# Optimization experiments

Hardware: AMD Instinct MI355X
Metric: run time of the kernel (lower is better)

## Reference

```python
import jax, jax.numpy as jnp
import numpy as np

B, NPER, H = 32, 512, 32
N, E = B * NPER, 65536
IN_CH, EDGE_CH, L1, L2, NL = 100, 16, 64, 64, 4


def setup_inputs() -> dict:
    key = jax.random.key(0)
    ks = jax.random.split(key, 14)
    f = lambda k, s: jax.random.normal(k, s, dtype=jnp.float32) * 0.1
    return {
        "x_nodes": jax.random.randint(ks[0], (N,), 0, IN_CH),
        "edge_index": jax.random.randint(ks[1], (2, E), 0, N),
        "edge_attr": jax.random.randint(ks[2], (E,), 0, EDGE_CH),
        "metal_idx": jax.random.randint(ks[3], (B,), 0, NPER),
        "loop_edge": jax.random.randint(ks[4], (B, L1, 2), 0, NPER),
        "loop_pair": jax.random.randint(ks[5], (B, L2, 2), 0, NPER),
        "node_emb": f(ks[6], (IN_CH, H)),
        "edge_emb": f(ks[7], (NL, EDGE_CH, 8)),
        "lin_w": f(ks[8], (NL, 8, H * H)),
        "lin_b": f(ks[9], (NL, H * H)),
        "root_w": f(ks[10], (NL, H, H)),
        "conv_b": f(ks[11], (NL, H)),
        "f_w": f(ks[12], (H, 1)),
        "f_b": f(ks[13], (1,)),
    }


def reference(x_nodes, edge_index, edge_attr, metal_idx, loop_edge, loop_pair,
              node_emb, edge_emb, lin_w, lin_b, root_w, conv_b, f_w, f_b):
    src, dst = edge_index[0], edge_index[1]
    # mean-aggregation denominator (clamped to 1 for isolated nodes, as PyG)
    deg = jax.ops.segment_sum(jnp.ones((E,), jnp.float32), dst, num_segments=N)
    denom = jnp.maximum(deg, 1.0)[:, None]

    x = node_emb[x_nodes]  # [N,H]
    for l in range(NL):
        # edge nn: Embedding -> ReLU -> Linear(8, H*H)
        e8 = jax.nn.relu(edge_emb[l][edge_attr])              # [E,8]
        W = (e8 @ lin_w[l] + lin_b[l]).reshape(E, H, H)       # [E,H,H]
        msg = jnp.einsum('ei,eio->eo', x[src], W)             # [E,H]
        agg = jax.ops.segment_sum(msg, dst, num_segments=N) / denom
        x_new = agg + x @ root_w[l] + conv_b[l]               # root weight + bias
        x = jax.nn.relu(x_new) if l < NL - 1 else x_new

    metal_g = metal_idx + jnp.arange(B) * NPER                # global metal node ids
    xm = x[metal_g]                                           # [B,H]
    fhM = (xm @ f_w + f_b)[:, 0]                              # [B]

    xg = x.reshape(B, NPER, H)
    bidx = jnp.arange(B)[:, None]

    def pair_prod(pairs):
        xs = xg[bidx, pairs[:, :, 0]]                         # [B,L,H]
        xt = xg[bidx, pairs[:, :, 1]]                         # [B,L,H]
        # sum(xm*xs) + sum(xm*xt) + sum(xs*(-xt))
        return jnp.sum(xm[:, None, :] * (xs + xt) - xs * xt, axis=-1)

    res_edge = pair_prod(loop_edge) - fhM[:, None]            # [B,L1]
    res_pair = -pair_prod(loop_pair)                          # [B,L2]
    return jnp.concatenate([res_edge, res_pair], axis=1)      # [B, L1+L2]
```

## Files before the change

kernel.cpp:

```cpp
#include <hip/hip_runtime.h>

#define NN 16384
#define NE 65536
#define H  32
#define BB 32
#define NPER 512
#define NL 4

__global__ void k_deg(const int* __restrict__ dst, float* __restrict__ deg) {
    int e = blockIdx.x * blockDim.x + threadIdx.x;
    if (e < NE) atomicAdd(&deg[dst[e]], 1.0f);
}

__global__ void k_embed(const int* __restrict__ x_nodes, const float* __restrict__ node_emb,
                        float* __restrict__ x) {
    int tid = blockIdx.x * blockDim.x + threadIdx.x;
    if (tid < NN * H) {
        int n = tid >> 5, h = tid & 31;
        x[tid] = node_emb[x_nodes[n] * H + h];
    }
}

__global__ void k_weights(const float* __restrict__ edge_emb_l, const float* __restrict__ lin_w_l,
                          const float* __restrict__ lin_b_l, float* __restrict__ Wt) {
    int tid = blockIdx.x * blockDim.x + threadIdx.x;
    if (tid < 16 * 1024) {
        int t = tid >> 10, io = tid & 1023;
        float acc = lin_b_l[io];
#pragma unroll
        for (int j = 0; j < 8; ++j) {
            float e = edge_emb_l[t * 8 + j];
            e = e > 0.f ? e : 0.f;
            acc += e * lin_w_l[j * 1024 + io];
        }
        Wt[tid] = acc;
    }
}

__global__ void k_msg(const int* __restrict__ src, const int* __restrict__ dst,
                      const int* __restrict__ eattr, const float* __restrict__ x,
                      const float* __restrict__ Wt, float* __restrict__ agg) {
    int tid = blockIdx.x * blockDim.x + threadIdx.x;
    int e = tid >> 5;
    int o = tid & 31;
    if (e >= NE) return;
    int s = src[e], d = dst[e], t = eattr[e];
    float xv = x[s * H + o];
    const float* __restrict__ W = Wt + t * 1024;
    int base = threadIdx.x & 32;
    float acc = 0.f;
#pragma unroll
    for (int i = 0; i < H; ++i) {
        float xi = __shfl(xv, base + i);
        acc += xi * W[i * H + o];
    }
    atomicAdd(&agg[d * H + o], acc);
}

__global__ void k_update(const float* __restrict__ x, const float* __restrict__ agg,
                         const float* __restrict__ deg, const float* __restrict__ root_w_l,
                         const float* __restrict__ conv_b_l, float* __restrict__ xout,
                         int do_relu) {
    int tid = blockIdx.x * blockDim.x + threadIdx.x;
    if (tid >= NN * H) return;
    int n = tid >> 5, o = tid & 31;
    float xv = x[tid];
    int base = threadIdx.x & 32;
    float acc = conv_b_l[o];
#pragma unroll
    for (int i = 0; i < H; ++i) {
        float xi = __shfl(xv, base + i);
        acc += xi * root_w_l[i * H + o];
    }
    float dg = deg[n];
    dg = dg < 1.f ? 1.f : dg;
    float v = agg[tid] / dg + acc;
    if (do_relu) v = v > 0.f ? v : 0.f;
    xout[tid] = v;
}

__global__ void k_final(const float* __restrict__ x, const int* __restrict__ metal_idx,
                        const int* __restrict__ loop_edge, const int* __restrict__ loop_pair,
                        const float* __restrict__ f_w, const float* __restrict__ f_b,
                        float* __restrict__ out) {
    int tid = blockIdx.x * blockDim.x + threadIdx.x;
    if (tid >= BB * 128) return;
    int b = tid >> 7, j = tid & 127;
    int mg = metal_idx[b] + b * NPER;
    const float* __restrict__ xm = x + mg * H;
    int p0, p1;
    if (j < 64) {
        p0 = loop_edge[(b * 64 + j) * 2];
        p1 = loop_edge[(b * 64 + j) * 2 + 1];
    } else {
        int j2 = j - 64;
        p0 = loop_pair[(b * 64 + j2) * 2];
        p1 = loop_pair[(b * 64 + j2) * 2 + 1];
    }
    const float* __restrict__ xs = x + (b * NPER + p0) * H;
    const float* __restrict__ xt = x + (b * NPER + p1) * H;
    float fh = f_b[0];
    float pp = 0.f;
#pragma unroll
    for (int h = 0; h < H; ++h) {
        float m = xm[h];
        fh += m * f_w[h];
        pp += m * (xs[h] + xt[h]) - xs[h] * xt[h];
    }
    out[tid] = (j < 64) ? (pp - fh) : (-pp);
}

extern "C" void kernel_launch(void* const* d_in, const int* in_sizes, int n_in,
                              void* d_out, int out_size, void* d_ws, size_t ws_size,
                              hipStream_t stream) {
    const int*   x_nodes    = (const int*)d_in[0];
    const int*   edge_index = (const int*)d_in[1];
    const int*   src        = edge_index;
    const int*   dst        = edge_index + NE;
    const int*   edge_attr  = (const int*)d_in[2];
    const int*   metal_idx  = (const int*)d_in[3];
    const int*   loop_edge  = (const int*)d_in[4];
    const int*   loop_pair  = (const int*)d_in[5];
    const float* node_emb   = (const float*)d_in[6];
    const float* edge_emb   = (const float*)d_in[7];
    const float* lin_w      = (const float*)d_in[8];
    const float* lin_b      = (const float*)d_in[9];
    const float* root_w     = (const float*)d_in[10];
    const float* conv_b     = (const float*)d_in[11];
    const float* f_w        = (const float*)d_in[12];
    const float* f_b        = (const float*)d_in[13];
    float* out = (float*)d_out;

    float* ws  = (float*)d_ws;
    float* xA  = ws;
    float* xB  = ws + NN * H;
    float* deg = ws + 2 * NN * H;
    float* Wt  = deg + NN;

    hipMemsetAsync(deg, 0, NN * sizeof(float), stream);
    k_deg<<<NE / 256, 256, 0, stream>>>(dst, deg);
    k_embed<<<NN * H / 256, 256, 0, stream>>>(x_nodes, node_emb, xA);

    float* xin = xA;
    float* xout = xB;
    for (int l = 0; l < NL; ++l) {
        k_weights<<<16 * 1024 / 256, 256, 0, stream>>>(
            edge_emb + l * 16 * 8, lin_w + l * 8 * 1024, lin_b + l * 1024, Wt);
        hipMemsetAsync(xout, 0, NN * H * sizeof(float), stream);
        k_msg<<<(NE * 32) / 256, 256, 0, stream>>>(src, dst, edge_attr, xin, Wt, xout);
        k_update<<<NN * H / 256, 256, 0, stream>>>(
            xin, xout, deg, root_w + l * H * H, conv_b + l * H, xout, l < NL - 1 ? 1 : 0);
        float* tmp = xin; xin = xout; xout = tmp;
    }

    k_final<<<(BB * 128 + 255) / 256, 256, 0, stream>>>(
        xin, metal_idx, loop_edge, loop_pair, f_w, f_b, out);
}
```

Before: 112.9 us.

## Build dst-sorted CSR once and fuse message aggregation with node update

Replaces per-layer edge-parallel atomic scatter with a CSR built once: a prep kernel fuses degree counting, embedding, and all-layer edge-weight precompute, then a single-block scan and a scatter build a destination-sorted packed edge list. Each layer becomes one kernel where a half-wave per node gathers incoming edges, applies the edge weight matrix, normalizes by degree, and adds the root transform. This removes float atomics, per-layer memsets, and several launches, but adds a serial single-block scan, and per-node work now varies with degree, so some waves sit idle while high-degree nodes finish.

```diff
diff --git a/kernel.cpp b/kernel.cpp
--- a/kernel.cpp
+++ b/kernel.cpp
@@ -7,74 +7,96 @@
 #define NPER 512
 #define NL 4
 
-__global__ void k_deg(const int* __restrict__ dst, float* __restrict__ deg) {
-    int e = blockIdx.x * blockDim.x + threadIdx.x;
-    if (e < NE) atomicAdd(&deg[dst[e]], 1.0f);
-}
+#define BLK_DEG 256
+#define BLK_EMB 2048
+#define BLK_W   256
 
-__global__ void k_embed(const int* __restrict__ x_nodes, const float* __restrict__ node_emb,
-                        float* __restrict__ x) {
-    int tid = blockIdx.x * blockDim.x + threadIdx.x;
-    if (tid < NN * H) {
+__global__ void k_prep(const int* __restrict__ dst, const int* __restrict__ x_nodes,
+                       const float* __restrict__ node_emb, const float* __restrict__ edge_emb,
+                       const float* __restrict__ lin_w, const float* __restrict__ lin_b,
+                       float* __restrict__ deg, float* __restrict__ x, float* __restrict__ Wt) {
+    int b = blockIdx.x;
+    if (b < BLK_DEG) {
+        int e = b * 256 + threadIdx.x;
+        atomicAdd(&deg[dst[e]], 1.0f);
+    } else if (b < BLK_DEG + BLK_EMB) {
+        int tid = (b - BLK_DEG) * 256 + threadIdx.x;
         int n = tid >> 5, h = tid & 31;
         x[tid] = node_emb[x_nodes[n] * H + h];
-    }
-}
-
-__global__ void k_weights(const float* __restrict__ edge_emb_l, const float* __restrict__ lin_w_l,
-                          const float* __restrict__ lin_b_l, float* __restrict__ Wt) {
-    int tid = blockIdx.x * blockDim.x + threadIdx.x;
-    if (tid < 16 * 1024) {
-        int t = tid >> 10, io = tid & 1023;
-        float acc = lin_b_l[io];
+    } else {
+        int tid = (b - BLK_DEG - BLK_EMB) * 256 + threadIdx.x;
+        int l = tid >> 14;
+        int rest = tid & 16383;
+        int t = rest >> 10, io = rest & 1023;
+        float acc = lin_b[l * 1024 + io];
 #pragma unroll
         for (int j = 0; j < 8; ++j) {
-            float e = edge_emb_l[t * 8 + j];
+            float e = edge_emb[(l * 16 + t) * 8 + j];
             e = e > 0.f ? e : 0.f;
-            acc += e * lin_w_l[j * 1024 + io];
+            acc += e * lin_w[(l * 8 + j) * 1024 + io];
         }
         Wt[tid] = acc;
     }
 }
 
-__global__ void k_msg(const int* __restrict__ src, const int* __restrict__ dst,
-                      const int* __restrict__ eattr, const float* __restrict__ x,
-                      const float* __restrict__ Wt, float* __restrict__ agg) {
-    int tid = blockIdx.x * blockDim.x + threadIdx.x;
-    int e = tid >> 5;
-    int o = tid & 31;
-    if (e >= NE) return;
-    int s = src[e], d = dst[e], t = eattr[e];
-    float xv = x[s * H + o];
-    const float* __restrict__ W = Wt + t * 1024;
-    int base = threadIdx.x & 32;
-    float acc = 0.f;
+__global__ void k_scan(const float* __restrict__ deg, int* __restrict__ offs) {
+    __shared__ int sums[1024];
+    int t = threadIdx.x;
+    int v[16];
+    int s = 0;
 #pragma unroll
-    for (int i = 0; i < H; ++i) {
-        float xi = __shfl(xv, base + i);
-        acc += xi * W[i * H + o];
+    for (int i = 0; i < 16; ++i) { v[i] = (int)deg[t * 16 + i]; s += v[i]; }
+    sums[t] = s;
+    __syncthreads();
+    for (int off = 1; off < 1024; off <<= 1) {
+        int a = (t >= off) ? sums[t - off] : 0;
+        __syncthreads();
+        sums[t] += a;
+        __syncthreads();
     }
-    atomicAdd(&agg[d * H + o], acc);
+    int run = (t > 0) ? sums[t - 1] : 0;
+#pragma unroll
+    for (int i = 0; i < 16; ++i) { offs[t * 16 + i] = run; run += v[i]; }
 }
 
-__global__ void k_update(const float* __restrict__ x, const float* __restrict__ agg,
-                         const float* __restrict__ deg, const float* __restrict__ root_w_l,
-                         const float* __restrict__ conv_b_l, float* __restrict__ xout,
-                         int do_relu) {
-    int tid = blockIdx.x * blockDim.x + threadIdx.x;
-    if (tid >= NN * H) return;
+__global__ void k_scatter(const int* __restrict__ src, const int* __restrict__ dst,
+                          const int* __restrict__ eattr, const int* __restrict__ offs,
+                          int* __restrict__ cnt, int* __restrict__ csr) {
+    int e = blockIdx.x * 256 + threadIdx.x;
+    int d = dst[e];
+    int slot = offs[d] + atomicAdd(&cnt[d], 1);
+    csr[slot] = src[e] | (eattr[e] << 14);
+}
+
+__global__ void k_layer(const float* __restrict__ xin, const int* __restrict__ offs,
+                        const int* __restrict__ csr, const float* __restrict__ deg,
+                        const float* __restrict__ Wt_l, const float* __restrict__ root_w_l,
+                        const float* __restrict__ conv_b_l, float* __restrict__ xout,
+                        int do_relu) {
+    int tid = blockIdx.x * 256 + threadIdx.x;
     int n = tid >> 5, o = tid & 31;
-    float xv = x[tid];
     int base = threadIdx.x & 32;
-    float acc = conv_b_l[o];
+    int e0 = offs[n];
+    float dg = deg[n];
+    int e1 = e0 + (int)dg;
+    float acc = 0.f;
+    for (int e = e0; e < e1; ++e) {
+        int packed = csr[e];
+        int s = packed & 16383;
+        int t = packed >> 14;
+        float xv = xin[s * H + o];
+        const float* __restrict__ W = Wt_l + t * 1024;
 #pragma unroll
-    for (int i = 0; i < H; ++i) {
-        float xi = __shfl(xv, base + i);
-        acc += xi * root_w_l[i * H + o];
+        for (int i = 0; i < H; ++i)
+            acc += __shfl(xv, base + i) * W[i * H + o];
     }
-    float dg = deg[n];
-    dg = dg < 1.f ? 1.f : dg;
-    float v = agg[tid] / dg + acc;
+    acc /= (dg < 1.f ? 1.f : dg);
+    float xs = xin[tid];
+    float accR = conv_b_l[o];
+#pragma unroll
+    for (int i = 0; i < H; ++i)
+        accR += __shfl(xs, base + i) * root_w_l[i * H + o];
+    float v = acc + accR;
     if (do_relu) v = v > 0.f ? v : 0.f;
     xout[tid] = v;
 }
@@ -131,25 +153,28 @@
     const float* f_b        = (const float*)d_in[13];
     float* out = (float*)d_out;
 
-    float* ws  = (float*)d_ws;
-    float* xA  = ws;
-    float* xB  = ws + NN * H;
-    float* deg = ws + 2 * NN * H;
-    float* Wt  = deg + NN;
+    float* ws   = (float*)d_ws;
+    float* xA   = ws;
+    float* xB   = xA + NN * H;
+    float* deg  = xB + NN * H;
+    int*   cnt  = (int*)(deg + NN);
+    int*   offs = cnt + NN;
+    int*   csr  = offs + NN;
+    float* Wt   = (float*)(csr + NE);
 
-    hipMemsetAsync(deg, 0, NN * sizeof(float), stream);
-    k_deg<<<NE / 256, 256, 0, stream>>>(dst, deg);
-    k_embed<<<NN * H / 256, 256, 0, stream>>>(x_nodes, node_emb, xA);
+    hipMemsetAsync(deg, 0, 2 * NN * sizeof(float), stream);
+
+    k_prep<<<BLK_DEG + BLK_EMB + BLK_W, 256, 0, stream>>>(
+        dst, x_nodes, node_emb, edge_emb, lin_w, lin_b, deg, xA, Wt);
+    k_scan<<<1, 1024, 0, stream>>>(deg, offs);
+    k_scatter<<<NE / 256, 256, 0, stream>>>(src, dst, edge_attr, offs, cnt, csr);
 
     float* xin = xA;
     float* xout = xB;
     for (int l = 0; l < NL; ++l) {
-        k_weights<<<16 * 1024 / 256, 256, 0, stream>>>(
-            edge_emb + l * 16 * 8, lin_w + l * 8 * 1024, lin_b + l * 1024, Wt);
-        hipMemsetAsync(xout, 0, NN * H * sizeof(float), stream);
-        k_msg<<<(NE * 32) / 256, 256, 0, stream>>>(src, dst, edge_attr, xin, Wt, xout);
-        k_update<<<NN * H / 256, 256, 0, stream>>>(
-            xin, xout, deg, root_w + l * H * H, conv_b + l * H, xout, l < NL - 1 ? 1 : 0);
+        k_layer<<<NN * H / 256, 256, 0, stream>>>(
+            xin, offs, csr, deg, Wt + l * 16 * 1024, root_w + l * H * H, conv_b + l * H,
+            xout, l < NL - 1 ? 1 : 0);
         float* tmp = xin; xin = xout; xout = tmp;
     }
 
```

After: 277.5 us. +145.9%, slower.

## Fuse GNN layers into per-layer kernels with packed edges and rotating buffers

Applied to the files above, without the earlier changes.

Merges embedding, all-layer weight generation, edge packing and degree counting into one prep kernel, and fuses message passing with the root/bias update into one kernel per layer. The update is now accumulated with atomics into a pre-zeroed buffer, ReLU is applied when the next layer reads its input, and a third rotating buffer is zeroed inside the same launch, replacing the per-layer memset. Edge src/dst/type are packed into one 32-bit word to cut index loads, and the mean division is folded into each message as a reciprocal multiply. This removes many launches and memsets. In exchange, the root-term writes become atomics and the floating-point summation order changes.

```diff
diff --git a/kernel.cpp b/kernel.cpp
--- a/kernel.cpp
+++ b/kernel.cpp
@@ -4,79 +4,78 @@
 #define NE 65536
 #define H  32
 #define BB 32
-#define NPER 512
-#define NL 4
+#define NPERB 512
 
-__global__ void k_deg(const int* __restrict__ dst, float* __restrict__ deg) {
-    int e = blockIdx.x * blockDim.x + threadIdx.x;
-    if (e < NE) atomicAdd(&deg[dst[e]], 1.0f);
-}
-
-__global__ void k_embed(const int* __restrict__ x_nodes, const float* __restrict__ node_emb,
-                        float* __restrict__ x) {
-    int tid = blockIdx.x * blockDim.x + threadIdx.x;
-    if (tid < NN * H) {
-        int n = tid >> 5, h = tid & 31;
-        x[tid] = node_emb[x_nodes[n] * H + h];
+__global__ void k_prep(const int* __restrict__ x_nodes, const int* __restrict__ edge_index,
+                       const int* __restrict__ edge_attr,
+                       const float* __restrict__ node_emb, const float* __restrict__ edge_emb,
+                       const float* __restrict__ lin_w, const float* __restrict__ lin_b,
+                       float* __restrict__ x0, float* __restrict__ Wt,
+                       unsigned int* __restrict__ packed, float* __restrict__ degf,
+                       float* __restrict__ zbuf) {
+    int t = blockIdx.x * 256 + threadIdx.x;
+    if (t < 524288) {
+        int n = t >> 5, h = t & 31;
+        x0[t] = node_emb[x_nodes[n] * H + h];
+    } else if (t < 589824) {
+        int w = t - 524288;
+        int l = w >> 14, rest = w & 16383;
+        int ty = rest >> 10, io = rest & 1023;
+        float acc = lin_b[l * 1024 + io];
+#pragma unroll
+        for (int j = 0; j < 8; ++j) {
+            float e = edge_emb[(l * 16 + ty) * 8 + j];
+            e = e > 0.f ? e : 0.f;
+            acc = fmaf(e, lin_w[(l * 8 + j) * 1024 + io], acc);
+        }
+        Wt[w] = acc;
+    } else if (t < 655360) {
+        int e = t - 589824;
+        unsigned int s  = (unsigned int)edge_index[e];
+        unsigned int d  = (unsigned int)edge_index[NE + e];
+        unsigned int ty = (unsigned int)edge_attr[e];
+        packed[e] = s | (d << 14) | (ty << 28);
+        atomicAdd(&degf[d], 1.0f);
+    } else {
+        zbuf[t - 655360] = 0.f;
     }
 }
 
-__global__ void k_weights(const float* __restrict__ edge_emb_l, const float* __restrict__ lin_w_l,
-                          const float* __restrict__ lin_b_l, float* __restrict__ Wt) {
-    int tid = blockIdx.x * blockDim.x + threadIdx.x;
-    if (tid < 16 * 1024) {
-        int t = tid >> 10, io = tid & 1023;
-        float acc = lin_b_l[io];
+__global__ void k_phase(const float* __restrict__ xin, float* __restrict__ xout,
+                        float* __restrict__ zbuf,
+                        const unsigned int* __restrict__ packed, const float* __restrict__ degf,
+                        const float* __restrict__ Wt_l, const float* __restrict__ root_l,
+                        const float* __restrict__ b_l, int relu_in) {
+    int t = blockIdx.x * 256 + threadIdx.x;
+    int base = threadIdx.x & 32;
+    if (t < 2097152) {
+        int e = t >> 5, o = t & 31;
+        unsigned int p = packed[e];
+        int s  = p & 16383;
+        int d  = (p >> 14) & 16383;
+        int ty = p >> 28;
+        float xv = xin[s * H + o];
+        if (relu_in) xv = xv > 0.f ? xv : 0.f;
+        float invd = __builtin_amdgcn_rcpf(fmaxf(degf[d], 1.0f));
+        const float* __restrict__ W = Wt_l + ty * 1024 + o;
+        float acc = 0.f;
 #pragma unroll
-        for (int j = 0; j < 8; ++j) {
-            float e = edge_emb_l[t * 8 + j];
-            e = e > 0.f ? e : 0.f;
-            acc += e * lin_w_l[j * 1024 + io];
-        }
-        Wt[tid] = acc;
+        for (int i = 0; i < 32; ++i)
+            acc = fmaf(__shfl(xv, base + i), W[i * 32], acc);
+        atomicAdd(&xout[d * H + o], acc * invd);
+    } else if (t < 2621440) {
+        int t2 = t - 2097152;
+        int o = t2 & 31;
+        float xv = xin[t2];
+        if (relu_in) xv = xv > 0.f ? xv : 0.f;
+        float acc = b_l[o];
+#pragma unroll
+        for (int i = 0; i < 32; ++i)
+            acc = fmaf(__shfl(xv, base + i), root_l[i * 32 + o], acc);
+        atomicAdd(&xout[t2], acc);
+    } else if (zbuf) {
+        zbuf[t - 2621440] = 0.f;
     }
-}
-
-__global__ void k_msg(const int* __restrict__ src, const int* __restrict__ dst,
-                      const int* __restrict__ eattr, const float* __restrict__ x,
-                      const float* __restrict__ Wt, float* __restrict__ agg) {
-    int tid = blockIdx.x * blockDim.x + threadIdx.x;
-    int e = tid >> 5;
-    int o = tid & 31;
-    if (e >= NE) return;
-    int s = src[e], d = dst[e], t = eattr[e];
-    float xv = x[s * H + o];
-    const float* __restrict__ W = Wt + t * 1024;
-    int base = threadIdx.x & 32;
-    float acc = 0.f;
-#pragma unroll
-    for (int i = 0; i < H; ++i) {
-        float xi = __shfl(xv, base + i);
-        acc += xi * W[i * H + o];
-    }
-    atomicAdd(&agg[d * H + o], acc);
-}
-
-__global__ void k_update(const float* __restrict__ x, const float* __restrict__ agg,
-                         const float* __restrict__ deg, const float* __restrict__ root_w_l,
-                         const float* __restrict__ conv_b_l, float* __restrict__ xout,
-                         int do_relu) {
-    int tid = blockIdx.x * blockDim.x + threadIdx.x;
-    if (tid >= NN * H) return;
-    int n = tid >> 5, o = tid & 31;
-    float xv = x[tid];
-    int base = threadIdx.x & 32;
-    float acc = conv_b_l[o];
-#pragma unroll
-    for (int i = 0; i < H; ++i) {
-        float xi = __shfl(xv, base + i);
-        acc += xi * root_w_l[i * H + o];
-    }
-    float dg = deg[n];
-    dg = dg < 1.f ? 1.f : dg;
-    float v = agg[tid] / dg + acc;
-    if (do_relu) v = v > 0.f ? v : 0.f;
-    xout[tid] = v;
 }
 
 __global__ void k_final(const float* __restrict__ x, const int* __restrict__ metal_idx,
@@ -86,7 +85,7 @@
     int tid = blockIdx.x * blockDim.x + threadIdx.x;
     if (tid >= BB * 128) return;
     int b = tid >> 7, j = tid & 127;
-    int mg = metal_idx[b] + b * NPER;
+    int mg = metal_idx[b] + b * NPERB;
     const float* __restrict__ xm = x + mg * H;
     int p0, p1;
     if (j < 64) {
@@ -97,14 +96,14 @@
         p0 = loop_pair[(b * 64 + j2) * 2];
         p1 = loop_pair[(b * 64 + j2) * 2 + 1];
     }
-    const float* __restrict__ xs = x + (b * NPER + p0) * H;
-    const float* __restrict__ xt = x + (b * NPER + p1) * H;
+    const float* __restrict__ xs = x + (b * NPERB + p0) * H;
+    const float* __restrict__ xt = x + (b * NPERB + p1) * H;
     float fh = f_b[0];
     float pp = 0.f;
 #pragma unroll
     for (int h = 0; h < H; ++h) {
         float m = xm[h];
-        fh += m * f_w[h];
+        fh = fmaf(m, f_w[h], fh);
         pp += m * (xs[h] + xt[h]) - xs[h] * xt[h];
     }
     out[tid] = (j < 64) ? (pp - fh) : (-pp);
@@ -115,8 +114,6 @@
                               hipStream_t stream) {
     const int*   x_nodes    = (const int*)d_in[0];
     const int*   edge_index = (const int*)d_in[1];
-    const int*   src        = edge_index;
-    const int*   dst        = edge_index + NE;
     const int*   edge_attr  = (const int*)d_in[2];
     const int*   metal_idx  = (const int*)d_in[3];
     const int*   loop_edge  = (const int*)d_in[4];
@@ -131,28 +128,27 @@
     const float* f_b        = (const float*)d_in[13];
     float* out = (float*)d_out;
 
-    float* ws  = (float*)d_ws;
-    float* xA  = ws;
-    float* xB  = ws + NN * H;
-    float* deg = ws + 2 * NN * H;
-    float* Wt  = deg + NN;
+    float* ws   = (float*)d_ws;
+    float* buf0 = ws;
+    float* buf1 = buf0 + NN * H;
+    float* buf2 = buf1 + NN * H;
+    float* degf = buf2 + NN * H;
+    unsigned int* packed = (unsigned int*)(degf + NN);
+    float* Wt   = (float*)(packed + NE);
 
-    hipMemsetAsync(deg, 0, NN * sizeof(float), stream);
-    k_deg<<<NE / 256, 256, 0, stream>>>(dst, deg);
-    k_embed<<<NN * H / 256, 256, 0, stream>>>(x_nodes, node_emb, xA);
+    hipMemsetAsync(degf, 0, NN * sizeof(float), stream);
 
-    float* xin = xA;
-    float* xout = xB;
-    for (int l = 0; l < NL; ++l) {
-        k_weights<<<16 * 1024 / 256, 256, 0, stream>>>(
-            edge_emb + l * 16 * 8, lin_w + l * 8 * 1024, lin_b + l * 1024, Wt);
-        hipMemsetAsync(xout, 0, NN * H * sizeof(float), stream);
-        k_msg<<<(NE * 32) / 256, 256, 0, stream>>>(src, dst, edge_attr, xin, Wt, xout);
-        k_update<<<NN * H / 256, 256, 0, stream>>>(
-            xin, xout, deg, root_w + l * H * H, conv_b + l * H, xout, l < NL - 1 ? 1 : 0);
-        float* tmp = xin; xin = xout; xout = tmp;
-    }
+    k_prep<<<4608, 256, 0, stream>>>(x_nodes, edge_index, edge_attr, node_emb, edge_emb,
+                                     lin_w, lin_b, buf0, Wt, packed, degf, buf1);
 
-    k_final<<<(BB * 128 + 255) / 256, 256, 0, stream>>>(
-        xin, metal_idx, loop_edge, loop_pair, f_w, f_b, out);
+    k_phase<<<12288, 256, 0, stream>>>(buf0, buf1, buf2, packed, degf,
+                                       Wt + 0 * 16384, root_w + 0 * 1024, conv_b + 0 * H, 0);
+    k_phase<<<12288, 256, 0, stream>>>(buf1, buf2, buf0, packed, degf,
+                                       Wt + 1 * 16384, root_w + 1 * 1024, conv_b + 1 * H, 1);
+    k_phase<<<12288, 256, 0, stream>>>(buf2, buf0, buf1, packed, degf,
+                                       Wt + 2 * 16384, root_w + 2 * 1024, conv_b + 2 * H, 1);
+    k_phase<<<10240, 256, 0, stream>>>(buf0, buf1, (float*)0, packed, degf,
+                                       Wt + 3 * 16384, root_w + 3 * 1024, conv_b + 3 * H, 1);
+
+    k_final<<<16, 256, 0, stream>>>(buf1, metal_idx, loop_edge, loop_pair, f_w, f_b, out);
 }
```

Measured after the change: 90.66 us. 1.24x faster.
